# Kernel tuning notes

Measured on AMD Instinct MI355X. Metric: run time of the kernel, lower is better.

Reference implementation:

```python
import jax, jax.numpy as jnp
import numpy as np

EPS = 1e-5

def _ln(x, g, b):
    mu = jnp.mean(x, axis=-1, keepdims=True)
    var = jnp.mean((x - mu) ** 2, axis=-1, keepdims=True)
    return (x - mu) * jax.lax.rsqrt(var + EPS) * g + b

def setup_inputs() -> dict:
    key = jax.random.key(0)
    ks = jax.random.split(key, 16)
    B, T, D, H = 64, 4096, 67, 128
    def lin(k, fi, fo):
        return jax.random.normal(k, (fi, fo), jnp.float32) / np.sqrt(fi)
    return {
        "x": jax.random.normal(ks[0], (B, T, D), jnp.float32),
        "dt": jax.random.uniform(ks[1], (B, T, 1), jnp.float32),
        "ln_in_g": jnp.ones((D,), jnp.float32),
        "ln_in_b": jnp.zeros((D,), jnp.float32),
        "proj_w": lin(ks[2], D, H),
        "proj_b": jnp.zeros((H,), jnp.float32),
        "ln_p_g": jnp.ones((H,), jnp.float32),
        "ln_p_b": jnp.zeros((H,), jnp.float32),
        "ff1_w": lin(ks[3], 2 * H, H),
        "ff1_b": jnp.zeros((H,), jnp.float32),
        "ff2_w": lin(ks[4], 2 * H, H),
        "ff2_b": jnp.zeros((H,), jnp.float32),
        "ta_w": lin(ks[5], 2 * H, H),
        "ta_b": jnp.zeros((H,), jnp.float32),
        "tb_w": lin(ks[6], 2 * H, H),
        "tb_b": jnp.zeros((H,), jnp.float32),
        "head_w": lin(ks[7], H, 1),
        "head_b": jnp.zeros((1,), jnp.float32),
    }

def reference(x, dt, ln_in_g, ln_in_b, proj_w, proj_b, ln_p_g, ln_p_b,
              ff1_w, ff1_b, ff2_w, ff2_b, ta_w, ta_b, tb_w, tb_b,
              head_w, head_b):
    B, T, _ = x.shape
    H = proj_w.shape[1]
    # input norm + feature projection (Linear -> LayerNorm -> SiLU)
    xn = _ln(x, ln_in_g, ln_in_b)
    feat = jax.nn.silu(_ln(jnp.einsum('btd,dh->bth', xn, proj_w) + proj_b, ln_p_g, ln_p_b))
    # CfC recurrence over time via scan
    feat_t = jnp.swapaxes(feat, 0, 1)          # [T,B,H]
    dt_t = jnp.swapaxes(dt, 0, 1) * 10.0       # [T,B,1]
    def step(h, inp):
        xt, dtt = inp
        cat = jnp.concatenate([xt, h], axis=-1)  # [B,2H]
        ff1 = jnp.tanh(cat @ ff1_w + ff1_b)
        ff2 = jnp.tanh(cat @ ff2_w + ff2_b)
        t_a = cat @ ta_w + ta_b
        t_b = cat @ tb_w + tb_b
        gate = jax.nn.sigmoid(t_a * dtt + t_b)
        h_new = ff1 * (1.0 - gate) + gate * ff2
        return h_new, h_new
    h0 = jnp.zeros((B, H), x.dtype)
    _, seq = jax.lax.scan(step, h0, (feat_t, dt_t))  # [T,B,H]
    seq = jnp.swapaxes(seq, 0, 1)                    # [B,T,H]
    logits = seq @ head_w + head_b                   # [B,T,1]
    return logits
```

## Files before the change

### kernel.cpp

```cpp
#include <hip/hip_runtime.h>
#include <cstdint>

#define Bb 64
#define Tt 4096
#define Dd 67
#define Hh 128
#define CH 16
#define NCH (Tt/CH)

typedef _Float16 f16;
typedef _Float16 half8 __attribute__((ext_vector_type(8)));
typedef float f32x4 __attribute__((ext_vector_type(4)));

#define MFMA16(A,B,C) __builtin_amdgcn_mfma_f32_16x16x32_f16((A),(B),(C),0,0,0)

static __device__ __forceinline__ float fast_rcp(float x){ return __builtin_amdgcn_rcpf(x); }
static __device__ __forceinline__ float fast_ex2(float x){ return __builtin_amdgcn_exp2f(x); }
static __device__ __forceinline__ float rlane(float v, int l){
  return __builtin_bit_cast(float, __builtin_amdgcn_readlane(__builtin_bit_cast(int, v), l));
}
#define L2E  1.442695041f
#define L2E2 2.885390082f

#define SYNC() do { asm volatile("s_waitcnt lgkmcnt(0)" ::: "memory"); \
                    __builtin_amdgcn_s_barrier(); } while(0)

union U2 { uint2 u; f16 h[4]; };
union U1 { unsigned u; f16 h[2]; };

__device__ __forceinline__ void red2(float& s, float& q){
#pragma unroll
  for (int off = 32; off; off >>= 1){ s += __shfl_xor(s, off); q += __shfl_xor(q, off); }
}

__global__ __launch_bounds__(512, 2)
void stage_a(const float* __restrict__ x,
             const float* __restrict__ g_in, const float* __restrict__ b_in,
             const float* __restrict__ proj_w, const float* __restrict__ proj_b,
             const float* __restrict__ g_p, const float* __restrict__ b_p,
             const float* __restrict__ w_ff1, const float* __restrict__ bi_ff1,
             const float* __restrict__ w_ff2, const float* __restrict__ bi_ff2,
             const float* __restrict__ w_ta,  const float* __restrict__ bi_ta,
             const float* __restrict__ w_tb,  const float* __restrict__ bi_tb,
             f16* __restrict__ zx)
{
  __shared__ __align__(16) f16   xn_s[16*104];
  __shared__ __align__(16) float fpre_s[16*132];
  __shared__ __align__(16) f16   feat_s[16*136];

  const int tid  = threadIdx.x;
  const int wv   = tid >> 6;
  const int lane = tid & 63;
  const int q    = lane >> 4;
  const int l16  = lane & 15;
  const int jq   = 16*wv + 4*q;

  const float* Wg[4] = { w_ff1, w_ff2, w_ta, w_tb };
  const float* Bg[4] = { bi_ff1, bi_ff2, bi_ta, bi_tb };

  half8 aW1[3];
#pragma unroll
  for (int c = 0; c < 3; ++c)
#pragma unroll
    for (int i = 0; i < 8; ++i){
      int k = 32*c + 8*q + i;
      aW1[c][i] = (k < Dd) ? (f16)proj_w[k*Hh + (16*wv + l16)] : (f16)0.f;
    }
  half8 aW2[4][4];
  f32x4 bias2[4];
#pragma unroll
  for (int g = 0; g < 4; ++g){
    const float* wp = Wg[g];
    const int jc = 16*wv + l16;
#pragma unroll
    for (int c = 0; c < 4; ++c)
#pragma unroll
      for (int i = 0; i < 8; ++i){
        int k = 32*c + 8*q + i;
        aW2[g][c][i] = (f16)wp[k*Hh + jc];
      }
    bias2[g] = *(const f32x4*)(Bg[g] + jq);
  }
  const float gi0 = g_in[lane], bi0 = b_in[lane];
  const float gi1 = (lane < 3) ? g_in[64+lane] : 0.f;
  const float bi1 = (lane < 3) ? b_in[64+lane] : 0.f;
  const float gp0 = g_p[lane],  bp0 = b_p[lane];
  const float gp1 = g_p[64+lane], bp1 = b_p[64+lane];
  const float pb0 = proj_b[lane], pb1 = proj_b[64+lane];

  for (int idx = tid; idx < 16*104; idx += 512)
    if ((idx % 104) >= Dd) xn_s[idx] = (f16)0.f;
  __syncthreads();

  const int wg   = blockIdx.x;
  const int b    = wg >> 2;
  const int t0wg = (wg & 3) * 1024;

  for (int it = 0; it < 64; ++it){
    const int tl0 = t0wg + it*16;
#pragma unroll
    for (int hf = 0; hf < 2; ++hf){
      const int ts = wv + 8*hf;
      const float* xr = x + (size_t)(b*Tt + tl0 + ts) * Dd;
      float v0 = xr[lane];
      float v1 = (lane < 3) ? xr[64+lane] : 0.f;
      float s = v0 + v1, qq = v0*v0 + v1*v1;
      red2(s, qq);
      float mu = s * (1.0f/Dd);
      float rstd = rsqrtf(qq * (1.0f/Dd) - mu*mu + 1e-5f);
      xn_s[ts*104 + lane] = (f16)((v0 - mu)*rstd*gi0 + bi0);
      if (lane < 3) xn_s[ts*104 + 64 + lane] = (f16)((v1 - mu)*rstd*gi1 + bi1);
    }
    __syncthreads();
    {
      f32x4 acc = {0.f, 0.f, 0.f, 0.f};
#pragma unroll
      for (int c = 0; c < 3; ++c){
        half8 bf = *(const half8*)(xn_s + l16*104 + 32*c + 8*q);
        acc = MFMA16(aW1[c], bf, acc);
      }
      *(f32x4*)(fpre_s + l16*132 + jq) = acc;
    }
    __syncthreads();
#pragma unroll
    for (int hf = 0; hf < 2; ++hf){
      const int ts = wv + 8*hf;
      float v0 = fpre_s[ts*132 + lane]      + pb0;
      float v1 = fpre_s[ts*132 + 64 + lane] + pb1;
      float s = v0 + v1, qq = v0*v0 + v1*v1;
      red2(s, qq);
      float mu = s * (1.0f/Hh);
      float rstd = rsqrtf(qq * (1.0f/Hh) - mu*mu + 1e-5f);
      float f0 = (v0 - mu)*rstd*gp0 + bp0;
      float f1 = (v1 - mu)*rstd*gp1 + bp1;
      f0 *= fast_rcp(1.0f + fast_ex2(-L2E*f0));
      f1 *= fast_rcp(1.0f + fast_ex2(-L2E*f1));
      feat_s[ts*136 + lane]      = (f16)f0;
      feat_s[ts*136 + 64 + lane] = (f16)f1;
    }
    __syncthreads();
    {
      half8 bf2[4];
#pragma unroll
      for (int c = 0; c < 4; ++c)
        bf2[c] = *(const half8*)(feat_s + l16*136 + 32*c + 8*q);
      const size_t trow = (size_t)(b*Tt + tl0 + l16) * 512;
      f32x4 accs2[4];
#pragma unroll
      for (int g = 0; g < 4; ++g){
        f32x4 acc = bias2[g];
#pragma unroll
        for (int c = 0; c < 4; ++c)
          acc = MFMA16(aW2[g][c], bf2[c], acc);
        accs2[g] = acc;
      }
#pragma unroll
      for (int r = 0; r < 4; ++r){
        U2 u;
#pragma unroll
        for (int g = 0; g < 4; ++g) u.h[g] = (f16)accs2[g][r];
        const int zoff = ((wv>>1)*128) + ((4*q + r)*8) + ((wv&1)*4);
        *(uint2*)(zx + trow + zoff) = u.u;
      }
    }
    __syncthreads();
  }
}

__global__ __launch_bounds__(512, 1)
void scan_k(f16* __restrict__ zx, const float* __restrict__ dt,
            const float* __restrict__ w_ff1, const float* __restrict__ w_ff2,
            const float* __restrict__ w_ta,  const float* __restrict__ w_tb)
{
  __shared__ __align__(16) f16 zbuf[2][CH*512];
  __shared__ __align__(16) f16 hist[CH][Hh];

  const int tid  = threadIdx.x;
  const int w8   = tid >> 6;
  const int lane = tid & 63;
  const int q    = lane >> 4;
  const int l16  = lane & 15;
  const int b    = blockIdx.x;

  const float* Wg[4] = { w_ff1, w_ff2, w_ta, w_tb };

  half8 bW[4][4];
#pragma unroll
  for (int g = 0; g < 4; ++g){
    const float* wp = Wg[g];
    const int jc = 16*w8 + l16;
#pragma unroll
    for (int c = 0; c < 4; ++c)
#pragma unroll
      for (int i = 0; i < 8; ++i)
        bW[g][c][i] = (f16)wp[(128 + 32*c + 8*q + i)*Hh + jc];
  }

  ((float2*)hist)[tid] = make_float2(0.f, 0.f);

  f16* zg = zx + (size_t)b*Tt*512;
  const float4* zg4 = (const float4*)zg;

  float4 rz[2];
  rz[0] = zg4[tid]; rz[1] = zg4[512 + tid];
  ((float4*)zbuf[0])[tid] = rz[0]; ((float4*)zbuf[0])[512 + tid] = rz[1];
  rz[0] = zg4[1024 + tid]; rz[1] = zg4[1536 + tid];
  float dtcur = dt[(size_t)b*Tt + l16] * 10.0f;
  __syncthreads();

  const f32x4 zero4 = {0.f, 0.f, 0.f, 0.f};
  const int zoff2 = (w8>>1)*128 + l16*8 + (w8&1)*4;

  for (int c = 0; c < NCH; ++c){
    const int cur = c & 1, nxt = cur ^ 1;
    ((float4*)zbuf[nxt])[tid] = rz[0];
    ((float4*)zbuf[nxt])[512 + tid] = rz[1];
    if (c + 2 < NCH){
      const float4* src = zg4 + (size_t)(c+2)*1024;
      rz[0] = src[tid]; rz[1] = src[512 + tid];
    }
    float dtnxt = dtcur;
    if (c + 1 < NCH) dtnxt = dt[(size_t)b*Tt + (c+1)*CH + l16] * 10.0f;
    const f16* zch = zbuf[cur];

    uint2 zv = *(const uint2*)(zch + zoff2);

#pragma unroll
    for (int st = 0; st < CH; ++st){
      const int slotR = (st + 15) & 15;
      half8 af[4];
#pragma unroll
      for (int cc = 0; cc < 4; ++cc)
        af[cc] = *(const half8*)(&hist[slotR][32*cc + 8*q]);
      U2 uz; uz.u = zv;
      const float dtt = rlane(dtcur, st);

      f32x4 pA[4], pB[4];
#pragma unroll
      for (int g = 0; g < 4; ++g) pA[g] = MFMA16(af[0], bW[g][0], zero4);
#pragma unroll
      for (int g = 0; g < 4; ++g) pB[g] = MFMA16(af[2], bW[g][2], zero4);
#pragma unroll
      for (int g = 0; g < 4; ++g) pA[g] = MFMA16(af[1], bW[g][1], pA[g]);
#pragma unroll
      for (int g = 0; g < 4; ++g) pB[g] = MFMA16(af[3], bW[g][3], pB[g]);

      if (st + 1 < CH) zv = *(const uint2*)(zch + (st+1)*512 + zoff2);

      float pre[4];
#pragma unroll
      for (int g = 0; g < 4; ++g)
        pre[g] = pA[g][0] + pB[g][0] + (float)uz.h[g];
      float gpre = __builtin_fmaf(pre[2], dtt, pre[3]);
      float g_ = fast_rcp(fast_ex2(-L2E*gpre) + 1.0f);
      float u_ = fast_rcp(fast_ex2(L2E2*pre[0]) + 1.0f);
      float v_ = fast_rcp(fast_ex2(L2E2*pre[1]) + 1.0f);
      float a_ = __builtin_fmaf(-2.0f, u_, 1.0f);
      float hn = __builtin_fmaf(2.0f*g_, u_ - v_, a_);
      if (q == 0)
        hist[st][16*w8 + l16] = (f16)hn;
      SYNC();
    }
    {
      const uint2 hv = ((const uint2*)hist)[tid];
      *(uint2*)(zg + ((size_t)(c*CH + (tid >> 5)))*512 + (size_t)(tid & 31)*4) = hv;
    }
    SYNC();
    dtcur = dtnxt;
  }
}

__global__ __launch_bounds__(256, 4)
void head_k(const f16* __restrict__ zx, const float* __restrict__ head_w,
            const float* __restrict__ head_b, float* __restrict__ out)
{
  const int tok  = (blockIdx.x << 2) + (threadIdx.x >> 6);
  const int lane = threadIdx.x & 63;
  U1 cv; cv.u = *(const unsigned*)(zx + (size_t)tok*512 + 2*lane);
  float s = (float)cv.h[0]*head_w[2*lane] + (float)cv.h[1]*head_w[2*lane+1];
#pragma unroll
  for (int off = 32; off; off >>= 1) s += __shfl_xor(s, off);
  if (lane == 0) out[tok] = s + head_b[0];
}

extern "C" void kernel_launch(void* const* d_in, const int* in_sizes, int n_in,
                              void* d_out, int out_size, void* d_ws, size_t ws_size,
                              hipStream_t stream)
{
  const float* x       = (const float*)d_in[0];
  const float* dt      = (const float*)d_in[1];
  const float* ln_in_g = (const float*)d_in[2];
  const float* ln_in_b = (const float*)d_in[3];
  const float* proj_w  = (const float*)d_in[4];
  const float* proj_b  = (const float*)d_in[5];
  const float* ln_p_g  = (const float*)d_in[6];
  const float* ln_p_b  = (const float*)d_in[7];
  const float* ff1_w   = (const float*)d_in[8];
  const float* ff1_b   = (const float*)d_in[9];
  const float* ff2_w   = (const float*)d_in[10];
  const float* ff2_b   = (const float*)d_in[11];
  const float* ta_w    = (const float*)d_in[12];
  const float* ta_b    = (const float*)d_in[13];
  const float* tb_w    = (const float*)d_in[14];
  const float* tb_b    = (const float*)d_in[15];
  const float* head_w  = (const float*)d_in[16];
  const float* head_b  = (const float*)d_in[17];

  f16*   zx  = (f16*)d_ws;
  float* out = (float*)d_out;

  stage_a<<<dim3(256), dim3(512), 0, stream>>>(
      x, ln_in_g, ln_in_b, proj_w, proj_b, ln_p_g, ln_p_b,
      ff1_w, ff1_b, ff2_w, ff2_b, ta_w, ta_b, tb_w, tb_b, zx);

  scan_k<<<dim3(Bb), dim3(512), 0, stream>>>(
      zx, dt, ff1_w, ff2_w, ta_w, tb_w);

  head_k<<<dim3(Bb*Tt/4), dim3(256), 0, stream>>>(
      zx, head_w, head_b, out);
}
```

Before: 2.285 ms.

## Prefetch next x rows, use lightweight barriers, fold z into MFMA accumulator, raise priority

The projection kernel now loads the next iteration's x rows into registers before working on the current ones, so global-load latency overlaps compute. It also swaps __syncthreads for the SYNC macro (lgkmcnt wait plus barrier). In the scan kernel the precomputed input contribution is placed in the initial MFMA accumulator instead of being added afterwards, and s_setprio is raised around the MFMA block to favour the serial recurrence path. The SYNC swap may be unsafe if it drops waits on global memory.

```diff
diff --git a/kernel.cpp b/kernel.cpp
--- a/kernel.cpp
+++ b/kernel.cpp
@@ -96,14 +96,32 @@
   const int b    = wg >> 2;
   const int t0wg = (wg & 3) * 1024;
 
+  float pv0[2], pv1[2];
+#pragma unroll
+  for (int hf = 0; hf < 2; ++hf){
+    const float* xr = x + (size_t)(b*Tt + t0wg + wv + 8*hf) * Dd;
+    pv0[hf] = xr[lane];
+    pv1[hf] = (lane < 3) ? xr[64+lane] : 0.f;
+  }
+
   for (int it = 0; it < 64; ++it){
     const int tl0 = t0wg + it*16;
+    float cv0[2] = { pv0[0], pv0[1] };
+    float cv1[2] = { pv1[0], pv1[1] };
+    if (it + 1 < 64){
+      const int tn = t0wg + (it+1)*16;
+#pragma unroll
+      for (int hf = 0; hf < 2; ++hf){
+        const float* xr = x + (size_t)(b*Tt + tn + wv + 8*hf) * Dd;
+        pv0[hf] = xr[lane];
+        pv1[hf] = (lane < 3) ? xr[64+lane] : 0.f;
+      }
+    }
 #pragma unroll
     for (int hf = 0; hf < 2; ++hf){
       const int ts = wv + 8*hf;
-      const float* xr = x + (size_t)(b*Tt + tl0 + ts) * Dd;
-      float v0 = xr[lane];
-      float v1 = (lane < 3) ? xr[64+lane] : 0.f;
+      float v0 = cv0[hf];
+      float v1 = cv1[hf];
       float s = v0 + v1, qq = v0*v0 + v1*v1;
       red2(s, qq);
       float mu = s * (1.0f/Dd);
@@ -111,7 +129,7 @@
       xn_s[ts*104 + lane] = (f16)((v0 - mu)*rstd*gi0 + bi0);
       if (lane < 3) xn_s[ts*104 + 64 + lane] = (f16)((v1 - mu)*rstd*gi1 + bi1);
     }
-    __syncthreads();
+    SYNC();
     {
       f32x4 acc = {0.f, 0.f, 0.f, 0.f};
 #pragma unroll
@@ -121,7 +139,7 @@
       }
       *(f32x4*)(fpre_s + l16*132 + jq) = acc;
     }
-    __syncthreads();
+    SYNC();
 #pragma unroll
     for (int hf = 0; hf < 2; ++hf){
       const int ts = wv + 8*hf;
@@ -138,7 +156,7 @@
       feat_s[ts*136 + lane]      = (f16)f0;
       feat_s[ts*136 + 64 + lane] = (f16)f1;
     }
-    __syncthreads();
+    SYNC();
     {
       half8 bf2[4];
 #pragma unroll
@@ -163,7 +181,7 @@
         *(uint2*)(zx + trow + zoff) = u.u;
       }
     }
-    __syncthreads();
+    SYNC();
   }
 }
 
@@ -235,26 +253,32 @@
       U2 uz; uz.u = zv;
       const float dtt = rlane(dtcur, st);
 
+      __builtin_amdgcn_s_setprio(1);
       f32x4 pA[4], pB[4];
 #pragma unroll
-      for (int g = 0; g < 4; ++g) pA[g] = MFMA16(af[0], bW[g][0], zero4);
+      for (int g = 0; g < 4; ++g){
+        f32x4 ci = zero4;
+        ci[0] = (float)uz.h[g];
+        pA[g] = MFMA16(af[0], bW[g][0], ci);
+      }
 #pragma unroll
       for (int g = 0; g < 4; ++g) pB[g] = MFMA16(af[2], bW[g][2], zero4);
 #pragma unroll
       for (int g = 0; g < 4; ++g) pA[g] = MFMA16(af[1], bW[g][1], pA[g]);
 #pragma unroll
       for (int g = 0; g < 4; ++g) pB[g] = MFMA16(af[3], bW[g][3], pB[g]);
+      __builtin_amdgcn_s_setprio(0);
 
       if (st + 1 < CH) zv = *(const uint2*)(zch + (st+1)*512 + zoff2);
 
-      float pre[4];
-#pragma unroll
-      for (int g = 0; g < 4; ++g)
-        pre[g] = pA[g][0] + pB[g][0] + (float)uz.h[g];
-      float gpre = __builtin_fmaf(pre[2], dtt, pre[3]);
+      float p0 = pA[0][0] + pB[0][0];
+      float p1 = pA[1][0] + pB[1][0];
+      float p2 = pA[2][0] + pB[2][0];
+      float p3 = pA[3][0] + pB[3][0];
+      float gpre = __builtin_fmaf(p2, dtt, p3);
       float g_ = fast_rcp(fast_ex2(-L2E*gpre) + 1.0f);
-      float u_ = fast_rcp(fast_ex2(L2E2*pre[0]) + 1.0f);
-      float v_ = fast_rcp(fast_ex2(L2E2*pre[1]) + 1.0f);
+      float u_ = fast_rcp(fast_ex2(L2E2*p0) + 1.0f);
+      float v_ = fast_rcp(fast_ex2(L2E2*p1) + 1.0f);
       float a_ = __builtin_fmaf(-2.0f, u_, 1.0f);
       float hn = __builtin_fmaf(2.0f*g_, u_ - v_, a_);
       if (q == 0)
@@ -262,8 +286,8 @@
       SYNC();
     }
     {
-      const uint2 hv = ((const uint2*)hist)[tid];
-      *(uint2*)(zg + ((size_t)(c*CH + (tid >> 5)))*512 + (size_t)(tid & 31)*4) = hv;
+      const uint2 hv2 = ((const uint2*)hist)[tid];
+      *(uint2*)(zg + ((size_t)(c*CH + (tid >> 5)))*512 + (size_t)(tid & 31)*4) = hv2;
     }
     SYNC();
     dtcur = dtnxt;
```

Result: faster. 2.238 ms (-2.0%).
